# Performance work log

Measured on AMD Instinct MI355X. Metric: run time of the kernel, lower is better.

The kernel has to match this reference:

```python
import jax, jax.numpy as jnp
import numpy as np

N = 8192
IN_F = 128
OUT_F = 64
ALPHA = 0.2  # LeakyReLU negative slope
EDGE_P = 0.02  # adjacency density
NEG_INF = -1e12


def setup_inputs() -> dict:
    key = jax.random.key(0)
    k1, k2, k3, k4 = jax.random.split(key, 4)
    input_h = jax.random.normal(k1, (N, IN_F), dtype=jnp.float32)
    # sparse-ish 0/1 adjacency mask, with self-loops so every softmax row is valid
    adj = (jax.random.uniform(k2, (N, N)) < EDGE_P).astype(jnp.float32)
    adj = adj + jnp.eye(N, dtype=jnp.float32)
    # xavier_uniform with gain 1.414 as in the torch init
    def xavier(k, shape, gain=1.414):
        fan_in, fan_out = shape[0], shape[1]
        bound = gain * np.sqrt(6.0 / (fan_in + fan_out))
        return jax.random.uniform(k, shape, jnp.float32, -bound, bound)
    W = xavier(k3, (IN_F, OUT_F))
    a = xavier(k4, (2 * OUT_F, 1))
    return {"input_h": input_h, "adj": adj, "W": W, "a": a}


def reference(input_h, adj, W, a):
    # Wh: [N, F]
    Wh = input_h @ W
    # e[i, j] = leakyrelu(a1 . Wh_i + a2 . Wh_j)  (decomposed, no N*N*2F concat)
    a1 = a[:OUT_F, 0]   # [F]
    a2 = a[OUT_F:, 0]   # [F]
    s_src = Wh @ a1     # [N]
    s_dst = Wh @ a2     # [N]
    e = jax.nn.leaky_relu(s_src[:, None] + s_dst[None, :], negative_slope=ALPHA)  # [N, N]
    att = jnp.where(adj > 0, e, NEG_INF)
    att = jax.nn.softmax(att, axis=1)
    # dropout is identity in eval mode (training=False)
    out_h = att @ Wh    # [N, F]
    return out_h
```

## Files before the change

kernel.cpp:

```cpp
#include <hip/hip_runtime.h>
#include <hip/hip_bf16.h>
#include <type_traits>

#define N 8192
#define IN_F 128
#define OUT_F 64
#define ALPHA 0.2f
#define LOG2E 1.442695040888963f
#define BUFN 512

__device__ __forceinline__ float cvt(float x) { return x; }
__device__ __forceinline__ float cvt(__hip_bfloat16 x) { return __bfloat162float(x); }

__device__ __forceinline__ bool probe_fp32(const void* adj) {
    unsigned int u = *(const unsigned int*)adj;
    return (u == 0x3F800000u) || (u == 0x40000000u);
}

template <typename T>
__device__ __forceinline__ void k1_body(
    const T* __restrict__ h, const T* __restrict__ W, const T* __restrict__ a,
    float* __restrict__ Wh, float* __restrict__ s_src, float* __restrict__ s_dst,
    float* Wf, float (*hrow)[IN_F])
{
    const int tid  = threadIdx.x;
    const int w    = tid >> 6;
    const int lane = tid & 63;

    for (int idx = tid; idx < IN_F * OUT_F; idx += 256)
        Wf[idx] = cvt(W[idx]);

    const int row0 = blockIdx.x * 4;
    for (int idx = tid; idx < 4 * IN_F; idx += 256) {
        int r = idx >> 7, c = idx & (IN_F - 1);
        hrow[r][c] = cvt(h[(size_t)(row0 + r) * IN_F + c]);
    }
    __syncthreads();

    const int i = row0 + w;
    float acc = 0.f;
    #pragma unroll 8
    for (int t = 0; t < IN_F; ++t)
        acc = fmaf(hrow[w][t], Wf[t * OUT_F + lane], acc);

    Wh[(size_t)i * OUT_F + lane] = acc;

    float s1 = acc * cvt(a[lane]);
    float s2 = acc * cvt(a[OUT_F + lane]);
    #pragma unroll
    for (int off = 32; off; off >>= 1) {
        s1 += __shfl_xor(s1, off, 64);
        s2 += __shfl_xor(s2, off, 64);
    }
    if (lane == 0) { s_src[i] = s1 * LOG2E; s_dst[i] = s2 * LOG2E; }
}

__global__ __launch_bounds__(256) void gat_k1(
    const void* h, const void* W, const void* a, const void* adj,
    float* Wh, float* s_src, float* s_dst)
{
    __shared__ float Wf[IN_F * OUT_F];
    __shared__ float hrow[4][IN_F];
    if (probe_fp32(adj))
        k1_body<float>((const float*)h, (const float*)W, (const float*)a,
                       Wh, s_src, s_dst, Wf, hrow);
    else
        k1_body<__hip_bfloat16>((const __hip_bfloat16*)h, (const __hip_bfloat16*)W,
                                (const __hip_bfloat16*)a, Wh, s_src, s_dst, Wf, hrow);
}

template <typename TADJ, bool OUT_F32>
__device__ __forceinline__ void k2_body(
    const TADJ* __restrict__ adj, const float* __restrict__ Wh,
    const float* __restrict__ s_src, const float* __restrict__ s_dstg,
    void* __restrict__ outv, float2 (*pbuf)[BUFN])
{
    const int tid  = threadIdx.x;
    const int w    = tid >> 6;
    const int lane = tid & 63;

    const int i = blockIdx.x * 4 + w;
    const float s_i = s_src[i];
    float2* buf = pbuf[w];

    int n = 0;

    auto issue = [&](int c, uint4& b0, uint4& b1, float4& s0, float4& s1) {
        const int jb = c * 512 + lane * 8;
        if constexpr (std::is_same<TADJ, float>::value) {
            const float* arow = adj + (size_t)i * N;
            b0 = *((const uint4*)(arow + jb));
            b1 = *((const uint4*)(arow + jb + 4));
        } else {
            const unsigned short* arow = (const unsigned short*)adj + (size_t)i * N;
            b0 = *((const uint4*)(arow + jb));
            (void)b1;
        }
        s0 = *((const float4*)(s_dstg + jb));
        s1 = *((const float4*)(s_dstg + jb + 4));
    };

    uint4  b0a, b1a; float4 s0a, s1a;
    uint4  b0b, b1b; float4 s0b, s1b;
    issue(0, b0a, b1a, s0a, s1a);

    for (int c = 0; c < 16; ++c) {
        if (c < 15) issue(c + 1, b0b, b1b, s0b, s1b);

        const int jb = c * 512 + lane * 8;

        unsigned int bits[8];
        if constexpr (std::is_same<TADJ, float>::value) {
            bits[0] = b0a.x; bits[1] = b0a.y; bits[2] = b0a.z; bits[3] = b0a.w;
            bits[4] = b1a.x; bits[5] = b1a.y; bits[6] = b1a.z; bits[7] = b1a.w;
        } else {
            bits[0] = b0a.x & 0xffffu; bits[1] = b0a.x >> 16;
            bits[2] = b0a.y & 0xffffu; bits[3] = b0a.y >> 16;
            bits[4] = b0a.z & 0xffffu; bits[5] = b0a.z >> 16;
            bits[6] = b0a.w & 0xffffu; bits[7] = b0a.w >> 16;
        }
        float sdv[8] = {s0a.x, s0a.y, s0a.z, s0a.w, s1a.x, s1a.y, s1a.z, s1a.w};

        #pragma unroll
        for (int t = 0; t < 8; ++t) {
            const bool nzt = (bits[t] != 0u);
            const unsigned long long m = __ballot(nzt);
            if (nzt) {
                int pre = __builtin_amdgcn_mbcnt_lo((unsigned int)m, 0);
                pre = __builtin_amdgcn_mbcnt_hi((unsigned int)(m >> 32), pre);
                buf[n + pre] = make_float2(s_i + sdv[t], __int_as_float(jb + t));
            }
            n += (int)__popcll(m);
        }

        b0a = b0b; b1a = b1b; s0a = s0b; s1a = s1b;
    }

    const int n8 = (n + 7) & ~7;
    if (lane < n8 - n) buf[n + lane] = make_float2(-1e30f, __int_as_float(0));
    __threadfence_block();

    float acc = 0.f, lsum = 0.f;
    for (int u = 0; u < n8; u += 8) {
        const float4 q0 = *((const float4*)&buf[u]);
        const float4 q1 = *((const float4*)&buf[u + 2]);
        const float4 q2 = *((const float4*)&buf[u + 4]);
        const float4 q3 = *((const float4*)&buf[u + 6]);
        const int j0 = __float_as_int(q0.y), j1 = __float_as_int(q0.w);
        const int j2 = __float_as_int(q1.y), j3 = __float_as_int(q1.w);
        const int j4 = __float_as_int(q2.y), j5 = __float_as_int(q2.w);
        const int j6 = __float_as_int(q3.y), j7 = __float_as_int(q3.w);

        const float w0 = Wh[((size_t)j0 << 6) + lane];
        const float w1 = Wh[((size_t)j1 << 6) + lane];
        const float w2 = Wh[((size_t)j2 << 6) + lane];
        const float w3 = Wh[((size_t)j3 << 6) + lane];
        const float w4 = Wh[((size_t)j4 << 6) + lane];
        const float w5 = Wh[((size_t)j5 << 6) + lane];
        const float w6 = Wh[((size_t)j6 << 6) + lane];
        const float w7 = Wh[((size_t)j7 << 6) + lane];

        const float p0 = __builtin_exp2f(fmaxf(q0.x, ALPHA * q0.x));
        const float p1 = __builtin_exp2f(fmaxf(q0.z, ALPHA * q0.z));
        const float p2 = __builtin_exp2f(fmaxf(q1.x, ALPHA * q1.x));
        const float p3 = __builtin_exp2f(fmaxf(q1.z, ALPHA * q1.z));
        const float p4 = __builtin_exp2f(fmaxf(q2.x, ALPHA * q2.x));
        const float p5 = __builtin_exp2f(fmaxf(q2.z, ALPHA * q2.z));
        const float p6 = __builtin_exp2f(fmaxf(q3.x, ALPHA * q3.x));
        const float p7 = __builtin_exp2f(fmaxf(q3.z, ALPHA * q3.z));

        lsum += ((p0 + p1) + (p2 + p3)) + ((p4 + p5) + (p6 + p7));

        acc = fmaf(p0, w0, acc);
        acc = fmaf(p1, w1, acc);
        acc = fmaf(p2, w2, acc);
        acc = fmaf(p3, w3, acc);
        acc = fmaf(p4, w4, acc);
        acc = fmaf(p5, w5, acc);
        acc = fmaf(p6, w6, acc);
        acc = fmaf(p7, w7, acc);
    }

    const float v = acc / lsum;
    if constexpr (OUT_F32)
        ((float*)outv)[(size_t)i * OUT_F + lane] = v;
    else
        ((__hip_bfloat16*)outv)[(size_t)i * OUT_F + lane] = __float2bfloat16(v);
}

__global__ __launch_bounds__(256) void gat_k2(
    const void* adj, const float* Wh, const float* s_src, const float* s_dst,
    void* out)
{
    __shared__ __align__(16) float2 pbuf[4][BUFN];
    if (probe_fp32(adj))
        k2_body<float, true>((const float*)adj, Wh, s_src, s_dst, out, pbuf);
    else
        k2_body<__hip_bfloat16, false>((const __hip_bfloat16*)adj, Wh, s_src, s_dst,
                                       out, pbuf);
}

extern "C" void kernel_launch(void* const* d_in, const int* in_sizes, int n_in,
                              void* d_out, int out_size, void* d_ws, size_t ws_size,
                              hipStream_t stream) {
    const void* h   = d_in[0];
    const void* adj = d_in[1];
    const void* W   = d_in[2];
    const void* a   = d_in[3];

    char* ws = (char*)d_ws;
    float* Wh    = (float*)ws;
    float* s_src = (float*)(ws + (size_t)N * OUT_F * 4);
    float* s_dst = s_src + N;

    gat_k1<<<N / 4, 256, 0, stream>>>(h, W, a, adj, Wh, s_src, s_dst);
    gat_k2<<<N / 4, 256, 0, stream>>>(adj, Wh, s_src, s_dst, d_out);
}
```

Baseline: 388.3 us.

## Compact neighbor indices via per-lane count ballots and gather s_dst later

After: 408.3 us. +5.1%, slower.

```diff
diff --git a/kernel.cpp b/kernel.cpp
--- a/kernel.cpp
+++ b/kernel.cpp
@@ -11,6 +11,11 @@
 
 __device__ __forceinline__ float cvt(float x) { return x; }
 __device__ __forceinline__ float cvt(__hip_bfloat16 x) { return __bfloat162float(x); }
+
+__device__ __forceinline__ int mbcnt64(unsigned long long m) {
+    int r = __builtin_amdgcn_mbcnt_lo((unsigned int)m, 0);
+    return __builtin_amdgcn_mbcnt_hi((unsigned int)(m >> 32), r);
+}
 
 __device__ __forceinline__ bool probe_fp32(const void* adj) {
     unsigned int u = *(const unsigned int*)adj;
@@ -73,7 +78,7 @@
 __device__ __forceinline__ void k2_body(
     const TADJ* __restrict__ adj, const float* __restrict__ Wh,
     const float* __restrict__ s_src, const float* __restrict__ s_dstg,
-    void* __restrict__ outv, float2 (*pbuf)[BUFN])
+    void* __restrict__ outv, int (*pbuf)[BUFN])
 {
     const int tid  = threadIdx.x;
     const int w    = tid >> 6;
@@ -81,11 +86,11 @@
 
     const int i = blockIdx.x * 4 + w;
     const float s_i = s_src[i];
-    float2* buf = pbuf[w];
+    int* buf = pbuf[w];
 
     int n = 0;
 
-    auto issue = [&](int c, uint4& b0, uint4& b1, float4& s0, float4& s1) {
+    auto issue = [&](int c, uint4& b0, uint4& b1) {
         const int jb = c * 512 + lane * 8;
         if constexpr (std::is_same<TADJ, float>::value) {
             const float* arow = adj + (size_t)i * N;
@@ -94,91 +99,86 @@
         } else {
             const unsigned short* arow = (const unsigned short*)adj + (size_t)i * N;
             b0 = *((const uint4*)(arow + jb));
-            (void)b1;
-        }
-        s0 = *((const float4*)(s_dstg + jb));
-        s1 = *((const float4*)(s_dstg + jb + 4));
+        }
     };
 
-    uint4  b0a, b1a; float4 s0a, s1a;
-    uint4  b0b, b1b; float4 s0b, s1b;
-    issue(0, b0a, b1a, s0a, s1a);
+    uint4 b0a, b1a, b0b, b1b;
+    issue(0, b0a, b1a);
 
     for (int c = 0; c < 16; ++c) {
-        if (c < 15) issue(c + 1, b0b, b1b, s0b, s1b);
+        if (c < 15) issue(c + 1, b0b, b1b);
 
         const int jb = c * 512 + lane * 8;
 
-        unsigned int bits[8];
+        unsigned int mask8 = 0;
         if constexpr (std::is_same<TADJ, float>::value) {
-            bits[0] = b0a.x; bits[1] = b0a.y; bits[2] = b0a.z; bits[3] = b0a.w;
-            bits[4] = b1a.x; bits[5] = b1a.y; bits[6] = b1a.z; bits[7] = b1a.w;
+            mask8 |= (b0a.x != 0u) ? 0x01u : 0u;
+            mask8 |= (b0a.y != 0u) ? 0x02u : 0u;
+            mask8 |= (b0a.z != 0u) ? 0x04u : 0u;
+            mask8 |= (b0a.w != 0u) ? 0x08u : 0u;
+            mask8 |= (b1a.x != 0u) ? 0x10u : 0u;
+            mask8 |= (b1a.y != 0u) ? 0x20u : 0u;
+            mask8 |= (b1a.z != 0u) ? 0x40u : 0u;
+            mask8 |= (b1a.w != 0u) ? 0x80u : 0u;
         } else {
-            bits[0] = b0a.x & 0xffffu; bits[1] = b0a.x >> 16;
-            bits[2] = b0a.y & 0xffffu; bits[3] = b0a.y >> 16;
-            bits[4] = b0a.z & 0xffffu; bits[5] = b0a.z >> 16;
-            bits[6] = b0a.w & 0xffffu; bits[7] = b0a.w >> 16;
-        }
-        float sdv[8] = {s0a.x, s0a.y, s0a.z, s0a.w, s1a.x, s1a.y, s1a.z, s1a.w};
-
+            mask8 |= ((b0a.x & 0xffffu) != 0u) ? 0x01u : 0u;
+            mask8 |= ((b0a.x >> 16)     != 0u) ? 0x02u : 0u;
+            mask8 |= ((b0a.y & 0xffffu) != 0u) ? 0x04u : 0u;
+            mask8 |= ((b0a.y >> 16)     != 0u) ? 0x08u : 0u;
+            mask8 |= ((b0a.z & 0xffffu) != 0u) ? 0x10u : 0u;
+            mask8 |= ((b0a.z >> 16)     != 0u) ? 0x20u : 0u;
+            mask8 |= ((b0a.w & 0xffffu) != 0u) ? 0x40u : 0u;
+            mask8 |= ((b0a.w >> 16)     != 0u) ? 0x80u : 0u;
+        }
+
+        const int cnt = __popc(mask8);
+        const unsigned long long m0 = __ballot((cnt >> 0) & 1);
+        const unsigned long long m1 = __ballot((cnt >> 1) & 1);
+        const unsigned long long m2 = __ballot((cnt >> 2) & 1);
+        const unsigned long long m3 = __ballot((cnt >> 3) & 1);
+        int pos = n + mbcnt64(m0) + 2 * mbcnt64(m1) + 4 * mbcnt64(m2) + 8 * mbcnt64(m3);
+        n += (int)__popcll(m0) + 2 * (int)__popcll(m1)
+           + 4 * (int)__popcll(m2) + 8 * (int)__popcll(m3);
+
+        unsigned int rem = mask8;
+        while (__any(rem != 0u)) {
+            if (rem) {
+                const int t = __ffs(rem) - 1;
+                buf[pos++] = jb + t;
+                rem &= rem - 1u;
+            }
+        }
+
+        b0a = b0b; b1a = b1b;
+    }
+
+    const int n8 = (n + 7) & ~7;
+    if (lane < n8 - n) buf[n + lane] = -1;
+    __threadfence_block();
+
+    float acc = 0.f, lsum = 0.f;
+    for (int u = 0; u < n8; u += 8) {
+        const int4 ja = *((const int4*)&buf[u]);
+        const int4 jb4 = *((const int4*)&buf[u + 4]);
+        const int js[8] = {ja.x, ja.y, ja.z, ja.w, jb4.x, jb4.y, jb4.z, jb4.w};
+
+        float sd[8], wv[8];
         #pragma unroll
         for (int t = 0; t < 8; ++t) {
-            const bool nzt = (bits[t] != 0u);
-            const unsigned long long m = __ballot(nzt);
-            if (nzt) {
-                int pre = __builtin_amdgcn_mbcnt_lo((unsigned int)m, 0);
-                pre = __builtin_amdgcn_mbcnt_hi((unsigned int)(m >> 32), pre);
-                buf[n + pre] = make_float2(s_i + sdv[t], __int_as_float(jb + t));
-            }
-            n += (int)__popcll(m);
-        }
-
-        b0a = b0b; b1a = b1b; s0a = s0b; s1a = s1b;
-    }
-
-    const int n8 = (n + 7) & ~7;
-    if (lane < n8 - n) buf[n + lane] = make_float2(-1e30f, __int_as_float(0));
-    __threadfence_block();
-
-    float acc = 0.f, lsum = 0.f;
-    for (int u = 0; u < n8; u += 8) {
-        const float4 q0 = *((const float4*)&buf[u]);
-        const float4 q1 = *((const float4*)&buf[u + 2]);
-        const float4 q2 = *((const float4*)&buf[u + 4]);
-        const float4 q3 = *((const float4*)&buf[u + 6]);
-        const int j0 = __float_as_int(q0.y), j1 = __float_as_int(q0.w);
-        const int j2 = __float_as_int(q1.y), j3 = __float_as_int(q1.w);
-        const int j4 = __float_as_int(q2.y), j5 = __float_as_int(q2.w);
-        const int j6 = __float_as_int(q3.y), j7 = __float_as_int(q3.w);
-
-        const float w0 = Wh[((size_t)j0 << 6) + lane];
-        const float w1 = Wh[((size_t)j1 << 6) + lane];
-        const float w2 = Wh[((size_t)j2 << 6) + lane];
-        const float w3 = Wh[((size_t)j3 << 6) + lane];
-        const float w4 = Wh[((size_t)j4 << 6) + lane];
-        const float w5 = Wh[((size_t)j5 << 6) + lane];
-        const float w6 = Wh[((size_t)j6 << 6) + lane];
-        const float w7 = Wh[((size_t)j7 << 6) + lane];
-
-        const float p0 = __builtin_exp2f(fmaxf(q0.x, ALPHA * q0.x));
-        const float p1 = __builtin_exp2f(fmaxf(q0.z, ALPHA * q0.z));
-        const float p2 = __builtin_exp2f(fmaxf(q1.x, ALPHA * q1.x));
-        const float p3 = __builtin_exp2f(fmaxf(q1.z, ALPHA * q1.z));
-        const float p4 = __builtin_exp2f(fmaxf(q2.x, ALPHA * q2.x));
-        const float p5 = __builtin_exp2f(fmaxf(q2.z, ALPHA * q2.z));
-        const float p6 = __builtin_exp2f(fmaxf(q3.x, ALPHA * q3.x));
-        const float p7 = __builtin_exp2f(fmaxf(q3.z, ALPHA * q3.z));
-
-        lsum += ((p0 + p1) + (p2 + p3)) + ((p4 + p5) + (p6 + p7));
-
-        acc = fmaf(p0, w0, acc);
-        acc = fmaf(p1, w1, acc);
-        acc = fmaf(p2, w2, acc);
-        acc = fmaf(p3, w3, acc);
-        acc = fmaf(p4, w4, acc);
-        acc = fmaf(p5, w5, acc);
-        acc = fmaf(p6, w6, acc);
-        acc = fmaf(p7, w7, acc);
+            const int jj = (js[t] < 0) ? 0 : js[t];
+            sd[t] = s_dstg[jj];
+            wv[t] = Wh[((size_t)jj << 6) + lane];
+        }
+
+        #pragma unroll
+        for (int t = 0; t < 8; ++t) {
+            float e = s_i + sd[t];
+            e = fmaxf(e, ALPHA * e);
+            const float pe = __builtin_exp2f(e);
+            const float p = (js[t] < 0) ? 0.f : pe;
+            lsum += p;
+            acc = fmaf(p, wv[t], acc);
+        }
     }
 
     const float v = acc / lsum;
@@ -192,7 +192,7 @@
     const void* adj, const float* Wh, const float* s_src, const float* s_dst,
     void* out)
 {
-    __shared__ __align__(16) float2 pbuf[4][BUFN];
+    __shared__ __align__(16) int pbuf[4][BUFN];
     if (probe_fp32(adj))
         k2_body<float, true>((const float*)adj, Wh, s_src, s_dst, out, pbuf);
     else
```
